# Optimization experiments

Hardware: AMD Instinct MI355X
Metric: run time of the kernel (lower is better)

## Reference

```python
import jax, jax.numpy as jnp
import numpy as np

B, NA, NB = 2, 2048, 2048
DIM_A, DIM_B = 256, 256
HEADS, DH_A, DH_B = 8, 64, 64
INNER_A, INNER_B = DH_A * HEADS, DH_B * HEADS
EPS = 1e-5


def layer_norm(x, w, b):
    m = jnp.mean(x, axis=-1, keepdims=True)
    v = jnp.mean(jnp.square(x - m), axis=-1, keepdims=True)
    return (x - m) * jax.lax.rsqrt(v + EPS) * w + b


def setup_inputs() -> dict:
    key = jax.random.key(0)
    ks = jax.random.split(key, 16)
    s = 0.02
    return {
        "feat_a": jax.random.normal(ks[0], (B, NA, DIM_A), jnp.float32),
        "feat_b": jax.random.normal(ks[1], (B, NB, DIM_B), jnp.float32),
        "mask_a_b": jax.random.bernoulli(ks[2], 0.5, (B, NA, NB)),
        # linear weights stored (in, out)
        "Wq": jax.random.normal(ks[3], (DIM_A, INNER_B), jnp.float32) * s,
        "bq": jnp.zeros((INNER_B,), jnp.float32),
        "Wk": jax.random.normal(ks[4], (DIM_B, INNER_B), jnp.float32) * s,
        "bk": jnp.zeros((INNER_B,), jnp.float32),
        "Wv": jax.random.normal(ks[5], (DIM_B, INNER_A), jnp.float32) * s,
        "bv": jnp.zeros((INNER_A,), jnp.float32),
        "Wg": jax.random.normal(ks[6], (DIM_A, INNER_A), jnp.float32) * s,
        "bg": jnp.zeros((INNER_A,), jnp.float32),
        "Wo": jax.random.normal(ks[7], (INNER_A, DIM_A), jnp.float32) * s,
        "bo": jnp.zeros((DIM_A,), jnp.float32),
        "ln_a_w": jnp.ones((DIM_A,), jnp.float32),
        "ln_a_b": jnp.zeros((DIM_A,), jnp.float32),
        "ln_b_w": jnp.ones((DIM_B,), jnp.float32),
        "ln_b_b": jnp.zeros((DIM_B,), jnp.float32),
        "qln_w": jnp.ones((INNER_B,), jnp.float32),
        "qln_b": jnp.zeros((INNER_B,), jnp.float32),
        "kln_w": jnp.ones((INNER_B,), jnp.float32),
        "kln_b": jnp.zeros((INNER_B,), jnp.float32),
    }


def reference(feat_a, feat_b, mask_a_b, Wq, bq, Wk, bk, Wv, bv, Wg, bg, Wo, bo,
              ln_a_w, ln_a_b, ln_b_w, ln_b_b, qln_w, qln_b, kln_w, kln_b):
    scale = DH_B ** -0.5
    fa = layer_norm(feat_a, ln_a_w, ln_a_b)            # (b, na, dim_a)
    fb = layer_norm(feat_b, ln_b_w, ln_b_b)            # (b, nb, dim_b)
    q = layer_norm(fa @ Wq + bq, qln_w, qln_b)         # (b, na, inner_b)
    k = layer_norm(fb @ Wk + bk, kln_w, kln_b)         # (b, nb, inner_b)
    v = fb @ Wv + bv                                   # (b, nb, inner_a)
    g = fa @ Wg + bg                                   # (b, na, inner_a)
    q = q.reshape(B, NA, HEADS, DH_B)
    k = k.reshape(B, NB, HEADS, DH_B)
    v = v.reshape(B, NB, HEADS, DH_A)
    g = g.reshape(B, NA, HEADS, DH_A)
    sim = jnp.einsum('bihd,bjhd->bhij', q, k) * scale  # (b, h, na, nb)
    neg = jnp.finfo(sim.dtype).min
    sim = jnp.where(mask_a_b[:, None, :, :], sim, neg)
    attn = jax.nn.softmax(sim, axis=-1)
    out = jnp.einsum('bhij,bjhd->bihd', attn, v)       # (b, na, h, dh_a)
    out = jax.nn.sigmoid(g) * out
    out = out.reshape(B, NA, INNER_A)
    return out @ Wo + bo                               # (b, na, dim_a)
```

## Files before the change

### kernel.cpp

```cpp
#include <hip/hip_runtime.h>
#include <hip/hip_bf16.h>

using bf16 = __hip_bfloat16;
typedef short bf16x8 __attribute__((ext_vector_type(8)));
typedef float f32x4 __attribute__((ext_vector_type(4)));
typedef unsigned short ushort8_t __attribute__((ext_vector_type(8)));
typedef unsigned uint4_t __attribute__((ext_vector_type(4)));
typedef unsigned uint2_t __attribute__((ext_vector_type(2)));
typedef unsigned long long u64;

static constexpr int NA_ = 2048, NB_ = 2048;
static constexpr int H_ = 8, DH_ = 64, INNER_ = 512;
static constexpr int MROWS = 2 * NA_;

#define MFMA32(a, b, c) __builtin_amdgcn_mfma_f32_16x16x32_bf16(a, b, c, 0, 0, 0)

#if __has_builtin(__builtin_amdgcn_exp2f)
#define EXP2(x) __builtin_amdgcn_exp2f(x)
#else
#define EXP2(x) exp2f(x)
#endif

__device__ __forceinline__ unsigned short bfbits(float x) {
  bf16 h = __float2bfloat16(x);
  return __builtin_bit_cast(unsigned short, h);
}
__device__ __forceinline__ float b2f(unsigned short u) {
  unsigned v = ((unsigned)u) << 16;
  return __builtin_bit_cast(float, v);
}

__device__ __forceinline__ unsigned pkbf(float a, float b) {
  unsigned ua = __builtin_bit_cast(unsigned, a) + 0x8000u;
  unsigned ub = __builtin_bit_cast(unsigned, b) + 0x8000u;
#if __has_builtin(__builtin_amdgcn_perm)
  return __builtin_amdgcn_perm(ub, ua, 0x07060302u);
#else
  return (ua >> 16) | (ub & 0xFFFF0000u);
#endif
}

__global__ __launch_bounds__(256) void prep_kernel(
    const float* __restrict__ fa_in, const float* __restrict__ fb_in,
    const float* __restrict__ law, const float* __restrict__ lab,
    const float* __restrict__ lbw, const float* __restrict__ lbb,
    bf16* __restrict__ fa, bf16* __restrict__ fb,
    const float* __restrict__ Wq, const float* __restrict__ Wk,
    const float* __restrict__ Wv, const float* __restrict__ Wg,
    const float* __restrict__ Wo,
    bf16* __restrict__ Wqt, bf16* __restrict__ Wkt,
    bf16* __restrict__ Wvt, bf16* __restrict__ Wgt,
    bf16* __restrict__ Woth, bf16* __restrict__ Wotl,
    const void* __restrict__ maskp, u64* __restrict__ mbits) {
  int blk = blockIdx.x;
  int t = threadIdx.x;
  if (blk < 2048) {
    int row = blk * 4 + (t >> 6);
    int lane = t & 63;
    const float *src, *w, *bb;
    bf16* dst;
    int r;
    if (row < MROWS) { src = fa_in; w = law; bb = lab; dst = fa; r = row; }
    else             { src = fb_in; w = lbw; bb = lbb; dst = fb; r = row - MROWS; }
    float4 x = *(const float4*)(src + (size_t)r * 256 + lane * 4);
    float s  = (x.x + x.y) + (x.z + x.w);
    float s2 = (x.x * x.x + x.y * x.y) + (x.z * x.z + x.w * x.w);
#pragma unroll
    for (int m = 32; m >= 1; m >>= 1) { s += __shfl_xor(s, m); s2 += __shfl_xor(s2, m); }
    float mean = s * (1.0f / 256.0f);
    float var  = s2 * (1.0f / 256.0f) - mean * mean;
    float rstd = rsqrtf(var + 1e-5f);
    float4 wv = *(const float4*)(w + lane * 4);
    float4 bv = *(const float4*)(bb + lane * 4);
    ushort4 o;
    o.x = bfbits((x.x - mean) * rstd * wv.x + bv.x);
    o.y = bfbits((x.y - mean) * rstd * wv.y + bv.y);
    o.z = bfbits((x.z - mean) * rstd * wv.z + bv.z);
    o.w = bfbits((x.w - mean) * rstd * wv.w + bv.w);
    *(ushort4*)(dst + (size_t)r * 256 + lane * 4) = o;
  } else if (blk < 4608) {
    int z = (blk - 2048) >> 9;
    int idx = ((blk - 2048) & 511) * 256 + t;
    if (z < 4) {
      const float* W = (z == 0) ? Wq : (z == 1) ? Wk : (z == 2) ? Wv : Wg;
      bf16* Wt = (z == 0) ? Wqt : (z == 1) ? Wkt : (z == 2) ? Wvt : Wgt;
      int kk = idx >> 9, n = idx & 511;
      Wt[n * 256 + kk] = __float2bfloat16(W[idx]);
    } else {
      int kk = idx >> 8, n = idx & 255;
      float w = Wo[idx];
      bf16 hi = __float2bfloat16(w);
      Woth[n * 512 + kk] = hi;
      Wotl[n * 512 + kk] = __float2bfloat16(w - __bfloat162float(hi));
    }
  } else {
    __shared__ unsigned shf[4];
    const unsigned char* mu = (const unsigned char*)maskp;
    bool nz = ((t & 3) != 0) && (mu[t] != 0);
    u64 bal = __ballot(nz);
    if ((t & 63) == 0) shf[t >> 6] = (bal != 0ull) ? 1u : 0u;
    __syncthreads();
    bool m8 = (shf[0] | shf[1] | shf[2] | shf[3]) != 0;
    int lane = t & 63, wid = t >> 6;
    int lb = blk - 4608;
    for (size_t word = (size_t)lb * 4 + wid; word < 131072; word += 8192) {
      size_t e = word * 64 + lane;
      int v = m8 ? (int)mu[e] : ((const int*)maskp)[e];
      u64 b2 = __ballot(v != 0);
      if (lane == 0) mbits[word] = b2;
    }
  }
}

__global__ __launch_bounds__(256) void gemm4_kernel(
    const bf16* __restrict__ fa, const bf16* __restrict__ fb,
    const bf16* __restrict__ Wqt, const bf16* __restrict__ Wkt,
    const bf16* __restrict__ Wgt, const bf16* __restrict__ Wvt,
    const float* __restrict__ bq, const float* __restrict__ bk,
    const float* __restrict__ bg, const float* __restrict__ bv,
    const float* __restrict__ qlw, const float* __restrict__ qlb,
    const float* __restrict__ klw, const float* __restrict__ klb,
    bf16* __restrict__ qo, bf16* __restrict__ ko,
    bf16* __restrict__ gout, bf16* __restrict__ vout) {
  __shared__ __align__(16) char sm[27648];
  int z = blockIdx.z;
  int t = threadIdx.x, wave = t >> 6, lane = t & 63;
  int lm = lane & 15, quad = lane >> 4, q8 = quad * 8;

  if (z < 2) {
    bf16* As = (bf16*)sm;
    float* Pred = (float*)(sm + 16896);
    float* MV   = (float*)(sm + 17408);
    const bf16* A    = z ? fb : fa;
    const bf16* Wt   = z ? Wkt : Wqt;
    const float* bias = z ? bk : bq;
    const float* lw  = z ? klw : qlw;
    const float* lb  = z ? klb : qlb;
    bf16* out        = z ? ko : qo;
    int m0 = blockIdx.x * 16;
#pragma unroll
    for (int i = 0; i < 2; i++) {
      int id = t + 256 * i, r = id >> 5, cg = id & 31;
      *(ushort8_t*)(&As[r * 264 + cg * 8]) =
          *(const ushort8_t*)(A + (size_t)(m0 + r) * 256 + cg * 8);
    }
    __syncthreads();
    int n0w = wave * 128;
    f32x4 acc[8] = {};
    const bf16* wrow[8];
#pragma unroll
    for (int ni = 0; ni < 8; ni++) wrow[ni] = Wt + (size_t)(n0w + ni * 16 + lm) * 256;
#pragma unroll
    for (int ks = 0; ks < 8; ks++) {
      int k0 = ks * 32;
      bf16x8 af = *(const bf16x8*)(&As[lm * 264 + k0 + q8]);
#pragma unroll
      for (int ni = 0; ni < 8; ni++) {
        bf16x8 bf_ = *(const bf16x8*)(wrow[ni] + k0 + q8);
        acc[ni] = MFMA32(af, bf_, acc[ni]);
      }
    }
    float bvv[8];
#pragma unroll
    for (int ni = 0; ni < 8; ni++) bvv[ni] = bias[n0w + ni * 16 + lm];
#pragma unroll
    for (int ni = 0; ni < 8; ni++)
#pragma unroll
      for (int r = 0; r < 4; r++) acc[ni][r] += bvv[ni];
#pragma unroll
    for (int r = 0; r < 4; r++) {
      float s = 0.f, s2 = 0.f;
#pragma unroll
      for (int ni = 0; ni < 8; ni++) { s += acc[ni][r]; s2 += acc[ni][r] * acc[ni][r]; }
#pragma unroll
      for (int m = 1; m <= 8; m <<= 1) { s += __shfl_xor(s, m); s2 += __shfl_xor(s2, m); }
      if (lm == 0) {
        int row = quad * 4 + r;
        Pred[row * 8 + wave * 2]     = s;
        Pred[row * 8 + wave * 2 + 1] = s2;
      }
    }
    __syncthreads();
    if (t < 16) {
      float s = 0.f, s2 = 0.f;
#pragma unroll
      for (int w = 0; w < 4; w++) { s += Pred[t * 8 + w * 2]; s2 += Pred[t * 8 + w * 2 + 1]; }
      float mean = s * (1.0f / 512.0f);
      float var  = s2 * (1.0f / 512.0f) - mean * mean;
      MV[t * 2]     = mean;
      MV[t * 2 + 1] = rsqrtf(var + 1e-5f);
    }
    __syncthreads();
    float lww[8], lbb_[8];
#pragma unroll
    for (int ni = 0; ni < 8; ni++) {
      lww[ni]  = lw[n0w + ni * 16 + lm];
      lbb_[ni] = lb[n0w + ni * 16 + lm];
    }
    if (z == 0) {
      const float SC = 0.125f * 1.44269504088896f;
#pragma unroll
      for (int ni = 0; ni < 8; ni++) { lww[ni] *= SC; lbb_[ni] *= SC; }
    }
#pragma unroll
    for (int r = 0; r < 4; r++) {
      int row = quad * 4 + r;
      float mean = MV[row * 2], rstd = MV[row * 2 + 1];
      size_t obase = (size_t)(m0 + row) * 512 + n0w;
#pragma unroll
      for (int ni = 0; ni < 8; ni++)
        out[obase + ni * 16 + lm] =
            __float2bfloat16((acc[ni][r] - mean) * rstd * lww[ni] + lbb_[ni]);
    }
  } else {
    bf16* As = (bf16*)sm;
    bf16* Bs = (bf16*)(sm + 18432);
    const bf16* A    = (z == 3) ? fb : fa;
    const bf16* Wt   = (z == 3) ? Wvt : Wgt;
    const float* bias = (z == 3) ? bv : bg;
    int x = blockIdx.x;
    int m0 = (x >> 3) * 128, n0 = (x & 7) * 64;
    int wm = wave * 32;
    f32x4 acc[2][4] = {};
    for (int k0 = 0; k0 < 256; k0 += 64) {
      __syncthreads();
#pragma unroll
      for (int i = 0; i < 4; i++) {
        int id = t + 256 * i, r = id >> 3, cg = id & 7;
        *(ushort8_t*)(&As[r * 72 + cg * 8]) =
            *(const ushort8_t*)(A + (size_t)(m0 + r) * 256 + k0 + cg * 8);
      }
#pragma unroll
      for (int i = 0; i < 2; i++) {
        int id = t + 256 * i, r = id >> 3, cg = id & 7;
        *(ushort8_t*)(&Bs[r * 72 + cg * 8]) =
            *(const ushort8_t*)(Wt + (size_t)(n0 + r) * 256 + k0 + cg * 8);
      }
      __syncthreads();
#pragma unroll
      for (int kk = 0; kk < 64; kk += 32) {
        bf16x8 af[2], bf_[4];
#pragma unroll
        for (int mi = 0; mi < 2; mi++)
          af[mi] = *(const bf16x8*)(&As[(wm + mi * 16 + lm) * 72 + kk + q8]);
#pragma unroll
        for (int ni = 0; ni < 4; ni++)
          bf_[ni] = *(const bf16x8*)(&Bs[(ni * 16 + lm) * 72 + kk + q8]);
#pragma unroll
        for (int mi = 0; mi < 2; mi++)
#pragma unroll
          for (int ni = 0; ni < 4; ni++)
            acc[mi][ni] = MFMA32(af[mi], bf_[ni], acc[mi][ni]);
      }
    }
    if (z == 2) {
#pragma unroll
      for (int mi = 0; mi < 2; mi++)
#pragma unroll
        for (int ni = 0; ni < 4; ni++) {
          int nn = n0 + ni * 16 + lm;
          float bvv = bias[nn];
          int mb = m0 + wm + mi * 16 + quad * 4;
#pragma unroll
          for (int r = 0; r < 4; r++)
            gout[(size_t)(mb + r) * 512 + nn] = __float2bfloat16(acc[mi][ni][r] + bvv);
        }
    } else {
      __syncthreads();
      bf16* buf = (bf16*)sm;
#pragma unroll
      for (int mi = 0; mi < 2; mi++)
#pragma unroll
        for (int ni = 0; ni < 4; ni++) {
          int d_local = ni * 16 + lm;
          float bvv = bias[n0 + d_local];
          int j_local = wm + mi * 16 + quad * 4;
#pragma unroll
          for (int r = 0; r < 4; r++)
            buf[d_local * 136 + j_local + r] = __float2bfloat16(acc[mi][ni][r] + bvv);
        }
      __syncthreads();
      int bidx2 = m0 >> 11, j0g = m0 & 2047, hh = n0 >> 6;
      int dl = t >> 2, jseg = (t & 3) * 32;
      bf16* dstrow = vout + (size_t)((bidx2 * 8 + hh) * 64 + dl) * 2048 + j0g + jseg;
#pragma unroll
      for (int c = 0; c < 4; c++)
        *(ushort8_t*)(dstrow + c * 8) = *(const ushort8_t*)(&buf[dl * 136 + jseg + c * 8]);
    }
  }
}

__global__ __launch_bounds__(512, 4) void attn_kernel(
    const bf16* __restrict__ q, const bf16* __restrict__ k,
    const bf16* __restrict__ vt, const bf16* __restrict__ g,
    const u64* __restrict__ mbits,
    bf16* __restrict__ gh, bf16* __restrict__ gl) {
  __shared__ __align__(16) char smem[46592];
  bf16* Qs = (bf16*)smem;
  bf16* KVB = (bf16*)(smem + 9216);
  float* Om = (float*)(smem + 9216);
  float* Lbuf = (float*)(smem + 46080);
  constexpr int BUFE = 2 * 64 * 72;

  int flat = blockIdx.y * 32 + blockIdx.x;
  int bh = (flat & 7) * 2 + (flat >> 8);
  int qt = (flat >> 3) & 31;
  int bidx = bh >> 3, h = bh & 7;
  int i0 = qt * 64;
  int t = threadIdx.x, wave = t >> 6, lane = t & 63;
  int wj = wave >> 2, wi = wave & 3;
  int lm = lane & 15, quad = lane >> 4, q8 = quad * 8;
  int wj32 = wj * 32, wi16 = wi * 16;
  int srow = t >> 3, scg = (t & 7) * 8;

  int sg = srow & 31;
  int ksrow = (srow & 32) + (((sg & 4) << 2) | ((sg & 24) >> 1) | (sg & 3));
  int ksl = ksrow * 72 + scg;
  int vsl = srow * 72 + scg;

  const bf16* kb = k + (size_t)(bidx * NB_) * INNER_ + h * DH_;
  const bf16* vb = vt + (size_t)(bh * DH_) * NB_;
  const bf16* ksrc = kb + (size_t)srow * INNER_ + scg;
  const bf16* vsrc = vb + (size_t)srow * NB_ + scg;

  *(ushort8_t*)(&Qs[srow * 72 + scg]) =
      *(const ushort8_t*)(q + (size_t)(bidx * NA_ + i0 + srow) * INNER_ + h * DH_ + scg);

  ushort8_t kr = *(const ushort8_t*)(ksrc);
  ushort8_t vr = *(const ushort8_t*)(vsrc);

  __syncthreads();
  bf16x8 bq0 = *(const bf16x8*)(&Qs[(wi16 + lm) * 72 + q8]);
  bf16x8 bq1 = *(const bf16x8*)(&Qs[(wi16 + lm) * 72 + 32 + q8]);

  *(ushort8_t*)(&KVB[ksl]) = kr;
  *(ushort8_t*)(&KVB[64 * 72 + vsl]) = vr;
  kr = *(const ushort8_t*)(ksrc + 64 * INNER_);
  vr = *(const ushort8_t*)(vsrc + 64);

  bf16x8 bone;
  {
    short onev = (lm == 0) ? (short)0x3F80 : (short)0;
#pragma unroll
    for (int i = 0; i < 8; i++) bone[i] = onev;
  }

  f32x4 oacc[4] = {};
  f32x4 lacc = {};

  const u64* mrp = mbits + (size_t)(bidx * NA_ + i0 + wi16 + lm) * (NB_ / 64);
  int shp = wj32 + quad * 8;
  u64 smw = mrp[0] >> shp;

  __syncthreads();

  for (int it = 0; it < 32; it++) {
    bf16* Ks = KVB + (it & 1) * BUFE;
    bf16* Vs = Ks + 64 * 72;
    if (it < 31) {
      bf16* Kn = KVB + ((it + 1) & 1) * BUFE;
      *(ushort8_t*)(&Kn[ksl]) = kr;
      *(ushort8_t*)(&Kn[64 * 72 + vsl]) = vr;
    }
    if (it < 30) {
      kr = *(const ushort8_t*)(ksrc + (size_t)(it + 2) * (64 * INNER_));
      vr = *(const ushort8_t*)(vsrc + (it + 2) * 64);
    }
    u64 nm = (it < 31) ? (mrp[it + 1] >> shp) : 0;

    bf16x8 a00 = *(const bf16x8*)(&Ks[(wj32 + lm) * 72 + q8]);
    bf16x8 a01 = *(const bf16x8*)(&Ks[(wj32 + lm) * 72 + 32 + q8]);
    bf16x8 a10 = *(const bf16x8*)(&Ks[(wj32 + 16 + lm) * 72 + q8]);
    bf16x8 a11 = *(const bf16x8*)(&Ks[(wj32 + 16 + lm) * 72 + 32 + q8]);
    f32x4 st0 = {0.f, 0.f, 0.f, 0.f}, st1 = {0.f, 0.f, 0.f, 0.f};
    st0 = MFMA32(a00, bq0, st0);
    st0 = MFMA32(a01, bq1, st0);
    st1 = MFMA32(a10, bq0, st1);
    st1 = MFMA32(a11, bq1, st1);

    float p0[4], p1[4];
#pragma unroll
    for (int r = 0; r < 4; r++) {
      bool l0 = (smw >> r) & 1ull;
      bool l1 = (smw >> (4 + r)) & 1ull;
      p0[r] = EXP2(l0 ? st0[r] : -200.0f);
      p1[r] = EXP2(l1 ? st1[r] : -200.0f);
    }

    uint4_t u0;
    u0[0] = pkbf(p0[0], p0[1]);
    u0[1] = pkbf(p0[2], p0[3]);
    u0[2] = pkbf(p1[0], p1[1]);
    u0[3] = pkbf(p1[2], p1[3]);
    bf16x8 pa = __builtin_bit_cast(bf16x8, u0);

#pragma unroll
    for (int c = 0; c < 4; c++) {
      bf16x8 v_ = *(const bf16x8*)(&Vs[(c * 16 + lm) * 72 + wj32 + q8]);
      oacc[c] = MFMA32(pa, v_, oacc[c]);
    }
    lacc = MFMA32(pa, bone, lacc);

    smw = nm;
    __syncthreads();
  }

  if (lm == 0) {
#pragma unroll
    for (int r = 0; r < 4; r++)
      Lbuf[wj * 64 + wi16 + quad * 4 + r] = lacc[r];
  }
  if (wj == 1) {
#pragma unroll
    for (int c = 0; c < 4; c++)
#pragma unroll
      for (int r = 0; r < 4; r++)
        Om[(wi16 + quad * 4 + r) * 66 + c * 16 + lm] = oacc[c][r];
  }
  __syncthreads();
  if (wj == 0) {
#pragma unroll
    for (int c = 0; c < 4; c++)
#pragma unroll
      for (int r = 0; r < 4; r++)
        Om[(wi16 + quad * 4 + r) * 66 + c * 16 + lm] += oacc[c][r];
  }
  __syncthreads();
  {
    int row = wave * 8 + (lane >> 3);
    int col = (lane & 7) * 8;
    float l = Lbuf[row] + Lbuf[64 + row];
    float inv = 1.0f / l;
    size_t idx = (size_t)(bidx * NA_ + i0 + row) * INNER_ + h * DH_ + col;
    ushort8_t gv = *(const ushort8_t*)(g + idx);
    ushort8_t oh, ol;
#pragma unroll
    for (int e = 0; e < 8; e++) {
      float o = Om[row * 66 + col + e];
      float gf = b2f((unsigned short)gv[e]);
      float sig = 1.0f / (1.0f + __expf(-gf));
      float val = o * inv * sig;
      unsigned short hb = bfbits(val);
      oh[e] = hb;
      ol[e] = bfbits(val - b2f(hb));
    }
    *(ushort8_t*)(gh + idx) = oh;
    *(ushort8_t*)(gl + idx) = ol;
  }
}

__global__ __launch_bounds__(256) void gemm_split_kernel(
    const bf16* __restrict__ Ah, const bf16* __restrict__ Al,
    const bf16* __restrict__ Bh, const bf16* __restrict__ Bl,
    const float* __restrict__ bias, float* __restrict__ C) {
  constexpr int K = 512, N = 256;
  __shared__ __align__(16) bf16 Ash[32 * 72];
  __shared__ __align__(16) bf16 Asl[32 * 72];
  __shared__ __align__(16) bf16 Bsh[64 * 72];
  __shared__ __align__(16) bf16 Bsl[64 * 72];
  int n0 = blockIdx.x * 64, m0 = blockIdx.y * 32;
  int t = threadIdx.x, wave = t >> 6, lane = t & 63;
  int lm = lane & 15, quad = lane >> 4, q8 = quad * 8;
  int wm = (wave & 1) * 16, wn = (wave >> 1) * 32;
  f32x4 acc[2] = {};
  for (int k0 = 0; k0 < K; k0 += 64) {
    __syncthreads();
    {
      int r = t >> 3, cg = t & 7;
      size_t ga = (size_t)(m0 + r) * K + k0 + cg * 8;
      *(ushort8_t*)(&Ash[r * 72 + cg * 8]) = *(const ushort8_t*)(Ah + ga);
      *(ushort8_t*)(&Asl[r * 72 + cg * 8]) = *(const ushort8_t*)(Al + ga);
    }
#pragma unroll
    for (int i = 0; i < 2; i++) {
      int id = t + 256 * i, r = id >> 3, cg = id & 7;
      size_t gb = (size_t)(n0 + r) * K + k0 + cg * 8;
      *(ushort8_t*)(&Bsh[r * 72 + cg * 8]) = *(const ushort8_t*)(Bh + gb);
      *(ushort8_t*)(&Bsl[r * 72 + cg * 8]) = *(const ushort8_t*)(Bl + gb);
    }
    __syncthreads();
#pragma unroll
    for (int kk = 0; kk < 64; kk += 32) {
      bf16x8 ah = *(const bf16x8*)(&Ash[(wm + lm) * 72 + kk + q8]);
      bf16x8 al = *(const bf16x8*)(&Asl[(wm + lm) * 72 + kk + q8]);
#pragma unroll
      for (int ni = 0; ni < 2; ni++) {
        bf16x8 bh_ = *(const bf16x8*)(&Bsh[(wn + ni * 16 + lm) * 72 + kk + q8]);
        bf16x8 bl_ = *(const bf16x8*)(&Bsl[(wn + ni * 16 + lm) * 72 + kk + q8]);
        acc[ni] = MFMA32(ah, bh_, acc[ni]);
        acc[ni] = MFMA32(ah, bl_, acc[ni]);
        acc[ni] = MFMA32(al, bh_, acc[ni]);
      }
    }
  }
#pragma unroll
  for (int ni = 0; ni < 2; ni++) {
    int n = n0 + wn + ni * 16 + lm;
    float bvv = bias[n];
    int mb = m0 + wm + quad * 4;
#pragma unroll
    for (int r = 0; r < 4; r++) C[(size_t)(mb + r) * N + n] = acc[ni][r] + bvv;
  }
}

extern "C" void kernel_launch(void* const* d_in, const int* in_sizes, int n_in,
                              void* d_out, int out_size, void* d_ws, size_t ws_size,
                              hipStream_t stream) {
  const float* feat_a = (const float*)d_in[0];
  const float* feat_b = (const float*)d_in[1];
  const void*  mask   = d_in[2];
  const float* Wq = (const float*)d_in[3];
  const float* bq = (const float*)d_in[4];
  const float* Wk = (const float*)d_in[5];
  const float* bk = (const float*)d_in[6];
  const float* Wv = (const float*)d_in[7];
  const float* bv = (const float*)d_in[8];
  const float* Wg = (const float*)d_in[9];
  const float* bg = (const float*)d_in[10];
  const float* Wo = (const float*)d_in[11];
  const float* bo = (const float*)d_in[12];
  const float* law = (const float*)d_in[13];
  const float* lab = (const float*)d_in[14];
  const float* lbw = (const float*)d_in[15];
  const float* lbb = (const float*)d_in[16];
  const float* qlw = (const float*)d_in[17];
  const float* qlb = (const float*)d_in[18];
  const float* klw = (const float*)d_in[19];
  const float* klb = (const float*)d_in[20];

  char* ws = (char*)d_ws;
  size_t off = 0;
  auto alloc = [&](size_t bytes) -> void* {
    void* p = ws + off;
    off += (bytes + 255) & ~(size_t)255;
    return p;
  };
  bf16* fa    = (bf16*)alloc((size_t)MROWS * 256 * 2);
  bf16* fb    = (bf16*)alloc((size_t)MROWS * 256 * 2);
  bf16* Wqt   = (bf16*)alloc((size_t)131072 * 2);
  bf16* Wkt   = (bf16*)alloc((size_t)131072 * 2);
  bf16* Wvt   = (bf16*)alloc((size_t)131072 * 2);
  bf16* Wgt   = (bf16*)alloc((size_t)131072 * 2);
  bf16* Woth  = (bf16*)alloc((size_t)131072 * 2);
  bf16* Wotl  = (bf16*)alloc((size_t)131072 * 2);
  bf16* qb_   = (bf16*)alloc((size_t)MROWS * 512 * 2);
  bf16* kb_   = (bf16*)alloc((size_t)MROWS * 512 * 2);
  bf16* vtb   = (bf16*)alloc((size_t)1024 * 2048 * 2);
  bf16* gbuf  = (bf16*)alloc((size_t)MROWS * 512 * 2);
  bf16* gh    = (bf16*)alloc((size_t)MROWS * 512 * 2);
  bf16* gl    = (bf16*)alloc((size_t)MROWS * 512 * 2);
  u64*  mbits = (u64*)alloc((size_t)131072 * 8);

  prep_kernel<<<6656, 256, 0, stream>>>(
      feat_a, feat_b, law, lab, lbw, lbb, fa, fb,
      Wq, Wk, Wv, Wg, Wo, Wqt, Wkt, Wvt, Wgt, Woth, Wotl, mask, mbits);
  gemm4_kernel<<<dim3(256, 1, 4), 256, 0, stream>>>(
      fa, fb, Wqt, Wkt, Wgt, Wvt, bq, bk, bg, bv,
      qlw, qlb, klw, klb, qb_, kb_, gbuf, vtb);
  attn_kernel<<<dim3(32, 16), 512, 0, stream>>>(qb_, kb_, vtb, gbuf, mbits, gh, gl);
  gemm_split_kernel<<<dim3(4, 128), 256, 0, stream>>>(gh, gl, Woth, Wotl, bo, (float*)d_out);
}
```

Baseline: 189.2 us.

## Halve attention query tile to 32 rows with 4 waves and more blocks

The attention kernel now uses 32-query tiles and 256-thread blocks, so it launches 1024 blocks instead of 512. This spreads the work better across the CUs. Q fragments are loaded straight from global memory into registers instead of being staged in shared memory. Each thread now loads two K and V rows per tile, and s_setprio hints are wrapped around the MFMA sections. In exchange, every K/V tile is fetched by twice as many blocks, which doubles the K/V traffic through global memory and L2.

Result: slower. 194.8 us (+3.0%).

```diff
diff --git a/kernel.cpp b/kernel.cpp
--- a/kernel.cpp
+++ b/kernel.cpp
@@ -6,7 +6,6 @@
 typedef float f32x4 __attribute__((ext_vector_type(4)));
 typedef unsigned short ushort8_t __attribute__((ext_vector_type(8)));
 typedef unsigned uint4_t __attribute__((ext_vector_type(4)));
-typedef unsigned uint2_t __attribute__((ext_vector_type(2)));
 typedef unsigned long long u64;
 
 static constexpr int NA_ = 2048, NB_ = 2048;
@@ -290,53 +289,45 @@
   }
 }
 
-__global__ __launch_bounds__(512, 4) void attn_kernel(
+__global__ __launch_bounds__(256, 4) void attn_kernel(
     const bf16* __restrict__ q, const bf16* __restrict__ k,
     const bf16* __restrict__ vt, const bf16* __restrict__ g,
     const u64* __restrict__ mbits,
     bf16* __restrict__ gh, bf16* __restrict__ gl) {
-  __shared__ __align__(16) char smem[46592];
-  bf16* Qs = (bf16*)smem;
-  bf16* KVB = (bf16*)(smem + 9216);
-  float* Om = (float*)(smem + 9216);
-  float* Lbuf = (float*)(smem + 46080);
-  constexpr int BUFE = 2 * 64 * 72;
-
-  int flat = blockIdx.y * 32 + blockIdx.x;
-  int bh = (flat & 7) * 2 + (flat >> 8);
-  int qt = (flat >> 3) & 31;
+  __shared__ __align__(16) char smem[37120];
+  bf16* KVB = (bf16*)smem;
+  float* Om = (float*)smem;
+  float* Lbuf = (float*)(smem + 36864);
+  constexpr int TILE = 64 * 72;
+  constexpr int BUFE = 2 * TILE;
+
+  int flat = blockIdx.y * 64 + blockIdx.x;
+  int bh = (flat & 7) * 2 + (flat >> 9);
+  int qt = (flat >> 3) & 63;
   int bidx = bh >> 3, h = bh & 7;
-  int i0 = qt * 64;
+  int i0 = qt * 32;
   int t = threadIdx.x, wave = t >> 6, lane = t & 63;
-  int wj = wave >> 2, wi = wave & 3;
+  int wj = wave >> 1, wi = wave & 1;
   int lm = lane & 15, quad = lane >> 4, q8 = quad * 8;
   int wj32 = wj * 32, wi16 = wi * 16;
   int srow = t >> 3, scg = (t & 7) * 8;
 
-  int sg = srow & 31;
-  int ksrow = (srow & 32) + (((sg & 4) << 2) | ((sg & 24) >> 1) | (sg & 3));
-  int ksl = ksrow * 72 + scg;
-  int vsl = srow * 72 + scg;
+  int ksrow = ((srow & 4) << 2) | ((srow & 24) >> 1) | (srow & 3);
+  int ksl0 = ksrow * 72 + scg;
+  int ksl1 = (ksrow + 32) * 72 + scg;
+  int vsl0 = TILE + srow * 72 + scg;
+  int vsl1 = TILE + (srow + 32) * 72 + scg;
 
   const bf16* kb = k + (size_t)(bidx * NB_) * INNER_ + h * DH_;
   const bf16* vb = vt + (size_t)(bh * DH_) * NB_;
-  const bf16* ksrc = kb + (size_t)srow * INNER_ + scg;
-  const bf16* vsrc = vb + (size_t)srow * NB_ + scg;
-
-  *(ushort8_t*)(&Qs[srow * 72 + scg]) =
-      *(const ushort8_t*)(q + (size_t)(bidx * NA_ + i0 + srow) * INNER_ + h * DH_ + scg);
-
-  ushort8_t kr = *(const ushort8_t*)(ksrc);
-  ushort8_t vr = *(const ushort8_t*)(vsrc);
-
-  __syncthreads();
-  bf16x8 bq0 = *(const bf16x8*)(&Qs[(wi16 + lm) * 72 + q8]);
-  bf16x8 bq1 = *(const bf16x8*)(&Qs[(wi16 + lm) * 72 + 32 + q8]);
-
-  *(ushort8_t*)(&KVB[ksl]) = kr;
-  *(ushort8_t*)(&KVB[64 * 72 + vsl]) = vr;
-  kr = *(const ushort8_t*)(ksrc + 64 * INNER_);
-  vr = *(const ushort8_t*)(vsrc + 64);
+  const bf16* ksrc0 = kb + (size_t)srow * INNER_ + scg;
+  const bf16* ksrc1 = kb + (size_t)(srow + 32) * INNER_ + scg;
+  const bf16* vsrc0 = vb + (size_t)srow * NB_ + scg;
+  const bf16* vsrc1 = vb + (size_t)(srow + 32) * NB_ + scg;
+
+  const bf16* qbase = q + (size_t)(bidx * NA_ + i0 + wi16 + lm) * INNER_ + h * DH_;
+  bf16x8 bq0 = *(const bf16x8*)(qbase + q8);
+  bf16x8 bq1 = *(const bf16x8*)(qbase + 32 + q8);
 
   bf16x8 bone;
   {
@@ -350,21 +341,37 @@
 
   const u64* mrp = mbits + (size_t)(bidx * NA_ + i0 + wi16 + lm) * (NB_ / 64);
   int shp = wj32 + quad * 8;
+
+  ushort8_t kr0 = *(const ushort8_t*)(ksrc0);
+  ushort8_t kr1 = *(const ushort8_t*)(ksrc1);
+  ushort8_t vr0 = *(const ushort8_t*)(vsrc0);
+  ushort8_t vr1 = *(const ushort8_t*)(vsrc1);
+  *(ushort8_t*)(&KVB[ksl0]) = kr0;
+  *(ushort8_t*)(&KVB[ksl1]) = kr1;
+  *(ushort8_t*)(&KVB[vsl0]) = vr0;
+  *(ushort8_t*)(&KVB[vsl1]) = vr1;
+  kr0 = *(const ushort8_t*)(ksrc0 + (size_t)64 * INNER_);
+  kr1 = *(const ushort8_t*)(ksrc1 + (size_t)64 * INNER_);
+  vr0 = *(const ushort8_t*)(vsrc0 + 64);
+  vr1 = *(const ushort8_t*)(vsrc1 + 64);
   u64 smw = mrp[0] >> shp;
-
   __syncthreads();
 
   for (int it = 0; it < 32; it++) {
     bf16* Ks = KVB + (it & 1) * BUFE;
-    bf16* Vs = Ks + 64 * 72;
+    bf16* Vs = Ks + TILE;
     if (it < 31) {
       bf16* Kn = KVB + ((it + 1) & 1) * BUFE;
-      *(ushort8_t*)(&Kn[ksl]) = kr;
-      *(ushort8_t*)(&Kn[64 * 72 + vsl]) = vr;
+      *(ushort8_t*)(&Kn[ksl0]) = kr0;
+      *(ushort8_t*)(&Kn[ksl1]) = kr1;
+      *(ushort8_t*)(&Kn[vsl0]) = vr0;
+      *(ushort8_t*)(&Kn[vsl1]) = vr1;
     }
     if (it < 30) {
-      kr = *(const ushort8_t*)(ksrc + (size_t)(it + 2) * (64 * INNER_));
-      vr = *(const ushort8_t*)(vsrc + (it + 2) * 64);
+      kr0 = *(const ushort8_t*)(ksrc0 + (size_t)(it + 2) * (64 * INNER_));
+      kr1 = *(const ushort8_t*)(ksrc1 + (size_t)(it + 2) * (64 * INNER_));
+      vr0 = *(const ushort8_t*)(vsrc0 + (it + 2) * 64);
+      vr1 = *(const ushort8_t*)(vsrc1 + (it + 2) * 64);
     }
     u64 nm = (it < 31) ? (mrp[it + 1] >> shp) : 0;
 
@@ -372,19 +379,19 @@
     bf16x8 a01 = *(const bf16x8*)(&Ks[(wj32 + lm) * 72 + 32 + q8]);
     bf16x8 a10 = *(const bf16x8*)(&Ks[(wj32 + 16 + lm) * 72 + q8]);
     bf16x8 a11 = *(const bf16x8*)(&Ks[(wj32 + 16 + lm) * 72 + 32 + q8]);
+    __builtin_amdgcn_s_setprio(1);
     f32x4 st0 = {0.f, 0.f, 0.f, 0.f}, st1 = {0.f, 0.f, 0.f, 0.f};
     st0 = MFMA32(a00, bq0, st0);
     st0 = MFMA32(a01, bq1, st0);
     st1 = MFMA32(a10, bq0, st1);
     st1 = MFMA32(a11, bq1, st1);
+    __builtin_amdgcn_s_setprio(0);
 
     float p0[4], p1[4];
 #pragma unroll
     for (int r = 0; r < 4; r++) {
-      bool l0 = (smw >> r) & 1ull;
-      bool l1 = (smw >> (4 + r)) & 1ull;
-      p0[r] = EXP2(l0 ? st0[r] : -200.0f);
-      p1[r] = EXP2(l1 ? st1[r] : -200.0f);
+      p0[r] = EXP2(((smw >> r) & 1ull) ? st0[r] : -200.0f);
+      p1[r] = EXP2(((smw >> (4 + r)) & 1ull) ? st1[r] : -200.0f);
     }
 
     uint4_t u0;
@@ -394,12 +401,14 @@
     u0[3] = pkbf(p1[2], p1[3]);
     bf16x8 pa = __builtin_bit_cast(bf16x8, u0);
 
+    __builtin_amdgcn_s_setprio(1);
 #pragma unroll
     for (int c = 0; c < 4; c++) {
       bf16x8 v_ = *(const bf16x8*)(&Vs[(c * 16 + lm) * 72 + wj32 + q8]);
       oacc[c] = MFMA32(pa, v_, oacc[c]);
     }
     lacc = MFMA32(pa, bone, lacc);
+    __builtin_amdgcn_s_setprio(0);
 
     smw = nm;
     __syncthreads();
@@ -408,7 +417,7 @@
   if (lm == 0) {
 #pragma unroll
     for (int r = 0; r < 4; r++)
-      Lbuf[wj * 64 + wi16 + quad * 4 + r] = lacc[r];
+      Lbuf[wj * 32 + wi16 + quad * 4 + r] = lacc[r];
   }
   if (wj == 1) {
 #pragma unroll
@@ -427,9 +436,9 @@
   }
   __syncthreads();
   {
-    int row = wave * 8 + (lane >> 3);
-    int col = (lane & 7) * 8;
-    float l = Lbuf[row] + Lbuf[64 + row];
+    int row = t >> 3;
+    int col = (t & 7) * 8;
+    float l = Lbuf[row] + Lbuf[32 + row];
     float inv = 1.0f / l;
     size_t idx = (size_t)(bidx * NA_ + i0 + row) * INNER_ + h * DH_ + col;
     ushort8_t gv = *(const ushort8_t*)(g + idx);
@@ -557,6 +566,6 @@
   gemm4_kernel<<<dim3(256, 1, 4), 256, 0, stream>>>(
       fa, fb, Wqt, Wkt, Wgt, Wvt, bq, bk, bg, bv,
       qlw, qlb, klw, klb, qb_, kb_, gbuf, vtb);
-  attn_kernel<<<dim3(32, 16), 512, 0, stream>>>(qb_, kb_, vtb, gbuf, mbits, gh, gl);
+  attn_kernel<<<dim3(64, 16), 256, 0, stream>>>(qb_, kb_, vtb, gbuf, mbits, gh, gl);
   gemm_split_kernel<<<dim3(4, 128), 256, 0, stream>>>(gh, gl, Woth, Wotl, bo, (float*)d_out);
 }
```

## Restructure output GEMM to stage full-K A rows and read B directly; add MFMA priority hints

Applied to the files above, without the earlier changes.

The output projection GEMM now loads a 16-row by 512 A tile (hi and lo split) into shared memory once and streams B fragments straight from global memory, with no per-K-step syncs. The tile shape changes to 16x128 with each wave owning 32 columns, and the grid changes to match. The attention loop also wraps its MFMA sections in s_setprio raise/lower calls so those waves get issue priority. The risk is that uncoalesced direct global B loads, now without LDS reuse across waves, cost more than the removed barriers.

Result: slower. 203.7 us (+7.6%).

```diff
diff --git a/kernel.cpp b/kernel.cpp
--- a/kernel.cpp
+++ b/kernel.cpp
@@ -6,7 +6,6 @@
 typedef float f32x4 __attribute__((ext_vector_type(4)));
 typedef unsigned short ushort8_t __attribute__((ext_vector_type(8)));
 typedef unsigned uint4_t __attribute__((ext_vector_type(4)));
-typedef unsigned uint2_t __attribute__((ext_vector_type(2)));
 typedef unsigned long long u64;
 
 static constexpr int NA_ = 2048, NB_ = 2048;
@@ -372,19 +371,19 @@
     bf16x8 a01 = *(const bf16x8*)(&Ks[(wj32 + lm) * 72 + 32 + q8]);
     bf16x8 a10 = *(const bf16x8*)(&Ks[(wj32 + 16 + lm) * 72 + q8]);
     bf16x8 a11 = *(const bf16x8*)(&Ks[(wj32 + 16 + lm) * 72 + 32 + q8]);
+    __builtin_amdgcn_s_setprio(1);
     f32x4 st0 = {0.f, 0.f, 0.f, 0.f}, st1 = {0.f, 0.f, 0.f, 0.f};
     st0 = MFMA32(a00, bq0, st0);
     st0 = MFMA32(a01, bq1, st0);
     st1 = MFMA32(a10, bq0, st1);
     st1 = MFMA32(a11, bq1, st1);
+    __builtin_amdgcn_s_setprio(0);
 
     float p0[4], p1[4];
 #pragma unroll
     for (int r = 0; r < 4; r++) {
-      bool l0 = (smw >> r) & 1ull;
-      bool l1 = (smw >> (4 + r)) & 1ull;
-      p0[r] = EXP2(l0 ? st0[r] : -200.0f);
-      p1[r] = EXP2(l1 ? st1[r] : -200.0f);
+      p0[r] = EXP2(((smw >> r) & 1ull) ? st0[r] : -200.0f);
+      p1[r] = EXP2(((smw >> (4 + r)) & 1ull) ? st1[r] : -200.0f);
     }
 
     uint4_t u0;
@@ -394,12 +393,14 @@
     u0[3] = pkbf(p1[2], p1[3]);
     bf16x8 pa = __builtin_bit_cast(bf16x8, u0);
 
+    __builtin_amdgcn_s_setprio(1);
 #pragma unroll
     for (int c = 0; c < 4; c++) {
       bf16x8 v_ = *(const bf16x8*)(&Vs[(c * 16 + lm) * 72 + wj32 + q8]);
       oacc[c] = MFMA32(pa, v_, oacc[c]);
     }
     lacc = MFMA32(pa, bone, lacc);
+    __builtin_amdgcn_s_setprio(0);
 
     smw = nm;
     __syncthreads();
@@ -454,50 +455,47 @@
     const bf16* __restrict__ Bh, const bf16* __restrict__ Bl,
     const float* __restrict__ bias, float* __restrict__ C) {
   constexpr int K = 512, N = 256;
-  __shared__ __align__(16) bf16 Ash[32 * 72];
-  __shared__ __align__(16) bf16 Asl[32 * 72];
-  __shared__ __align__(16) bf16 Bsh[64 * 72];
-  __shared__ __align__(16) bf16 Bsl[64 * 72];
-  int n0 = blockIdx.x * 64, m0 = blockIdx.y * 32;
+  __shared__ __align__(16) bf16 Ash[16 * 520];
+  __shared__ __align__(16) bf16 Asl[16 * 520];
+  int n0 = blockIdx.x * 128, m0 = blockIdx.y * 16;
   int t = threadIdx.x, wave = t >> 6, lane = t & 63;
   int lm = lane & 15, quad = lane >> 4, q8 = quad * 8;
-  int wm = (wave & 1) * 16, wn = (wave >> 1) * 32;
+#pragma unroll
+  for (int i = 0; i < 4; i++) {
+    int id = t + 256 * i, r = id >> 6, cg = id & 63;
+    size_t ga = (size_t)(m0 + r) * K + cg * 8;
+    *(ushort8_t*)(&Ash[r * 520 + cg * 8]) = *(const ushort8_t*)(Ah + ga);
+    *(ushort8_t*)(&Asl[r * 520 + cg * 8]) = *(const ushort8_t*)(Al + ga);
+  }
+  __syncthreads();
+  int n0w = n0 + wave * 32;
   f32x4 acc[2] = {};
-  for (int k0 = 0; k0 < K; k0 += 64) {
-    __syncthreads();
-    {
-      int r = t >> 3, cg = t & 7;
-      size_t ga = (size_t)(m0 + r) * K + k0 + cg * 8;
-      *(ushort8_t*)(&Ash[r * 72 + cg * 8]) = *(const ushort8_t*)(Ah + ga);
-      *(ushort8_t*)(&Asl[r * 72 + cg * 8]) = *(const ushort8_t*)(Al + ga);
-    }
-#pragma unroll
-    for (int i = 0; i < 2; i++) {
-      int id = t + 256 * i, r = id >> 3, cg = id & 7;
-      size_t gb = (size_t)(n0 + r) * K + k0 + cg * 8;
-      *(ushort8_t*)(&Bsh[r * 72 + cg * 8]) = *(const ushort8_t*)(Bh + gb);
-      *(ushort8_t*)(&Bsl[r * 72 + cg * 8]) = *(const ushort8_t*)(Bl + gb);
-    }
-    __syncthreads();
-#pragma unroll
-    for (int kk = 0; kk < 64; kk += 32) {
-      bf16x8 ah = *(const bf16x8*)(&Ash[(wm + lm) * 72 + kk + q8]);
-      bf16x8 al = *(const bf16x8*)(&Asl[(wm + lm) * 72 + kk + q8]);
-#pragma unroll
-      for (int ni = 0; ni < 2; ni++) {
-        bf16x8 bh_ = *(const bf16x8*)(&Bsh[(wn + ni * 16 + lm) * 72 + kk + q8]);
-        bf16x8 bl_ = *(const bf16x8*)(&Bsl[(wn + ni * 16 + lm) * 72 + kk + q8]);
-        acc[ni] = MFMA32(ah, bh_, acc[ni]);
-        acc[ni] = MFMA32(ah, bl_, acc[ni]);
-        acc[ni] = MFMA32(al, bh_, acc[ni]);
-      }
-    }
-  }
+  const bf16* bhrow[2];
+  const bf16* blrow[2];
 #pragma unroll
   for (int ni = 0; ni < 2; ni++) {
-    int n = n0 + wn + ni * 16 + lm;
+    bhrow[ni] = Bh + (size_t)(n0w + ni * 16 + lm) * K;
+    blrow[ni] = Bl + (size_t)(n0w + ni * 16 + lm) * K;
+  }
+#pragma unroll
+  for (int ks = 0; ks < 16; ks++) {
+    int k0 = ks * 32;
+    bf16x8 ah = *(const bf16x8*)(&Ash[lm * 520 + k0 + q8]);
+    bf16x8 al = *(const bf16x8*)(&Asl[lm * 520 + k0 + q8]);
+#pragma unroll
+    for (int ni = 0; ni < 2; ni++) {
+      bf16x8 bh_ = *(const bf16x8*)(bhrow[ni] + k0 + q8);
+      bf16x8 bl_ = *(const bf16x8*)(blrow[ni] + k0 + q8);
+      acc[ni] = MFMA32(ah, bh_, acc[ni]);
+      acc[ni] = MFMA32(ah, bl_, acc[ni]);
+      acc[ni] = MFMA32(al, bh_, acc[ni]);
+    }
+  }
+#pragma unroll
+  for (int ni = 0; ni < 2; ni++) {
+    int n = n0w + ni * 16 + lm;
     float bvv = bias[n];
-    int mb = m0 + wm + quad * 4;
+    int mb = m0 + quad * 4;
 #pragma unroll
     for (int r = 0; r < 4; r++) C[(size_t)(mb + r) * N + n] = acc[ni][r] + bvv;
   }
@@ -558,5 +556,5 @@
       fa, fb, Wqt, Wkt, Wgt, Wvt, bq, bk, bg, bv,
       qlw, qlb, klw, klb, qb_, kb_, gbuf, vtb);
   attn_kernel<<<dim3(32, 16), 512, 0, stream>>>(qb_, kb_, vtb, gbuf, mbits, gh, gl);
-  gemm_split_kernel<<<dim3(4, 128), 256, 0, stream>>>(gh, gl, Woth, Wotl, bo, (float*)d_out);
-}
+  gemm_split_kernel<<<dim3(2, 256), 256, 0, stream>>>(gh, gl, Woth, Wotl, bo, (float*)d_out);
+}
```
